# Performance work log

Hardware: AMD Instinct MI355X
Metric: run time of the kernel (lower is better)

The kernel has to match this reference:

```python
import jax, jax.numpy as jnp
import numpy as np
from jax import lax

IN_CH = 256
NUM_CLASSES = 21
ROI = 7
SCALE = 1.0 / 32
SR = 2  # sampling_ratio
B = 2
NPROP = 128
FH = FW = 32
IMG = 1024
SCORE_THRESH = 0.05
NMS_THRESH = 0.5
MAX_DET = 100


def setup_inputs() -> dict:
    key = jax.random.key(0)
    ks = jax.random.split(key, 10)
    features = jax.random.normal(ks[0], (B, IN_CH, FH, FW), jnp.float32)
    x1 = jax.random.uniform(ks[1], (B, NPROP), minval=0.0, maxval=IMG - 160.0)
    y1 = jax.random.uniform(ks[2], (B, NPROP), minval=0.0, maxval=IMG - 160.0)
    w = jax.random.uniform(ks[3], (B, NPROP), minval=32.0, maxval=160.0)
    h = jax.random.uniform(ks[4], (B, NPROP), minval=32.0, maxval=160.0)
    proposals = jnp.stack([x1, y1, x1 + w, y1 + h], axis=-1)  # [B, NPROP, 4]
    img_sizes = jnp.full((B, 2), IMG, dtype=jnp.int32)  # (h, w)
    feat_dim = IN_CH * ROI * ROI

    def kaiming(k, shape):
        return jax.random.normal(k, shape, jnp.float32) * np.float32(np.sqrt(2.0 / shape[1]))

    W1 = kaiming(ks[5], (1024, feat_dim)); b1 = jnp.zeros((1024,), jnp.float32)
    W2 = kaiming(ks[6], (1024, 1024)); b2 = jnp.zeros((1024,), jnp.float32)
    Wc = jax.random.normal(ks[7], (NUM_CLASSES, 1024), jnp.float32) * 0.01
    bc = jnp.zeros((NUM_CLASSES,), jnp.float32)
    Wb = jax.random.normal(ks[8], (NUM_CLASSES * 4, 1024), jnp.float32) * 0.001
    bb = jnp.zeros((NUM_CLASSES * 4,), jnp.float32)
    return dict(features=features, proposals=proposals, img_sizes=img_sizes,
                W1=W1, b1=b1, W2=W2, b2=b2, Wc=Wc, bc=bc, Wb=Wb, bb=bb)


def roi_align(features, bidx, rois):
    """torchvision-style RoIAlign (aligned=False), spatial_scale=SCALE, sampling_ratio=SR.
    features [B,C,H,W], bidx [N] int, rois [N,4] -> [N, C*ROI*ROI] (channel-major flatten)."""
    Bf, C, H, W = features.shape
    x1 = rois[:, 0] * SCALE; y1 = rois[:, 1] * SCALE
    x2 = rois[:, 2] * SCALE; y2 = rois[:, 3] * SCALE
    rw = jnp.maximum(x2 - x1, 1.0); rh = jnp.maximum(y2 - y1, 1.0)
    bw = rw / ROI; bh = rh / ROI
    # per-bin sample offsets: [ROI, SR]
    g = jnp.arange(ROI, dtype=jnp.float32)[:, None] + (jnp.arange(SR, dtype=jnp.float32)[None, :] + 0.5) / SR
    ys = y1[:, None, None] + g[None] * bh[:, None, None]  # [N, ROI, SR]
    xs = x1[:, None, None] + g[None] * bw[:, None, None]  # [N, ROI, SR]
    y = ys[:, :, :, None, None]  # [N,ph,sy,1,1]
    x = xs[:, None, None, :, :]  # [N,1,1,pw,sx]
    inb = (y >= -1.0) & (y <= H) & (x >= -1.0) & (x <= W)  # [N,ph,sy,pw,sx]
    yc = jnp.clip(y, 0.0, H - 1.0); xc = jnp.clip(x, 0.0, W - 1.0)
    y0f = jnp.floor(yc); x0f = jnp.floor(xc)
    y0 = y0f.astype(jnp.int32); x0 = x0f.astype(jnp.int32)
    y1i = jnp.minimum(y0 + 1, H - 1); x1i = jnp.minimum(x0 + 1, W - 1)
    ly = yc - y0f; lx = xc - x0f
    hy = 1.0 - ly; hx = 1.0 - lx
    b = bidx[:, None, None, None, None]
    # gather four corners: advanced indices broadcast -> [N,ph,sy,pw,sx,C]
    f00 = features[b, :, y0, x0]
    f01 = features[b, :, y0, x1i]
    f10 = features[b, :, y1i, x0]
    f11 = features[b, :, y1i, x1i]
    val = ((hy * hx)[..., None] * f00 + (hy * lx)[..., None] * f01
           + (ly * hx)[..., None] * f10 + (ly * lx)[..., None] * f11)
    val = val * inb[..., None]
    pooled = val.mean(axis=(2, 4))            # [N, ph, pw, C]
    pooled = jnp.transpose(pooled, (0, 3, 1, 2))  # [N, C, ph, pw] (torch layout)
    return pooled.reshape(pooled.shape[0], -1)


def decode_boxes(deltas, props):
    pw = props[..., 2] - props[..., 0]
    ph = props[..., 3] - props[..., 1]
    px = props[..., 0] + pw / 2
    py = props[..., 1] + ph / 2
    cx = px + deltas[..., 0] * pw
    cy = py + deltas[..., 1] * ph
    w = pw * jnp.exp(deltas[..., 2])
    h = ph * jnp.exp(deltas[..., 3])
    return jnp.stack([cx - w / 2, cy - h / 2, cx + w / 2, cy + h / 2], axis=-1)


def nms_fixed(boxes, scores, valid, iou_thresh, max_out):
    """Greedy NMS with fixed shapes. Returns (indices[max_out], ok_mask[max_out])."""
    M = scores.shape[0]
    s = jnp.where(valid, scores, -jnp.inf)
    order = jnp.argsort(-s)
    b = boxes[order]; v = valid[order]
    bx1, by1, bx2, by2 = b[:, 0], b[:, 1], b[:, 2], b[:, 3]
    area = (bx2 - bx1) * (by2 - by1)
    idxs = jnp.arange(M)

    def body(i, keep):
        xi1 = jnp.maximum(bx1[i], bx1); yi1 = jnp.maximum(by1[i], by1)
        xi2 = jnp.minimum(bx2[i], bx2); yi2 = jnp.minimum(by2[i], by2)
        inter = jnp.maximum(xi2 - xi1, 0.0) * jnp.maximum(yi2 - yi1, 0.0)
        iou = inter / (area[i] + area - inter + 1e-9)
        suppress = (iou > iou_thresh) & (idxs > i)
        return jnp.where(keep[i], keep & ~suppress, keep)

    keep = lax.fori_loop(0, M, body, v)
    pos = jnp.where(keep, idxs, M)
    take = jnp.sort(pos)[:max_out]
    ok = take < M
    take = jnp.where(ok, take, 0)
    return order[take], ok


def postprocess_image(probs, reg, props, img_hw):
    Ncls = probs.shape[1]
    scores = probs[:, 1:]                    # [N, C-1] (skip background)
    deltas = reg[:, 1:, :]                   # [N, C-1, 4]
    boxes = decode_boxes(deltas, props[:, None, :])  # [N, C-1, 4]
    h = img_hw[0].astype(boxes.dtype); w = img_hw[1].astype(boxes.dtype)
    boxes = jnp.stack([jnp.clip(boxes[..., 0], 0.0, w), jnp.clip(boxes[..., 1], 0.0, h),
                       jnp.clip(boxes[..., 2], 0.0, w), jnp.clip(boxes[..., 3], 0.0, h)], axis=-1)
    labels = jnp.broadcast_to(jnp.arange(1, Ncls, dtype=jnp.int32)[None, :], scores.shape)
    fb = boxes.reshape(-1, 4); fs = scores.reshape(-1); fl = labels.reshape(-1)
    valid = fs > SCORE_THRESH
    maxc = jnp.max(jnp.where(valid, jnp.max(fb, axis=1), 0.0))
    off = fl.astype(fb.dtype) * (maxc + 1.0)
    zero = jnp.zeros_like(off)
    fb_off = fb + jnp.stack([off, zero, off, zero], axis=-1)
    idx, ok = nms_fixed(fb_off, fs, valid, NMS_THRESH, MAX_DET)
    m = ok.astype(fb.dtype)
    return fb[idx] * m[:, None], fs[idx] * m, fl[idx] * ok.astype(jnp.int32)


def reference(features, proposals, img_sizes, W1, b1, W2, b2, Wc, bc, Wb, bb):
    Bn, NP = proposals.shape[0], proposals.shape[1]
    bidx = jnp.repeat(jnp.arange(Bn, dtype=jnp.int32), NP)
    props_flat = proposals.reshape(-1, 4)
    roi_feats = roi_align(features, bidx, props_flat)       # [N, C*49]
    x = jax.nn.relu(roi_feats @ W1.T + b1)
    x = jax.nn.relu(x @ W2.T + b2)
    cls_logits = x @ Wc.T + bc                              # [N, NUM_CLASSES]
    box_reg = (x @ Wb.T + bb).reshape(-1, NUM_CLASSES, 4)   # [N, NUM_CLASSES, 4]
    probs = jax.nn.softmax(cls_logits, axis=-1)
    out_b, out_s, out_l = [], [], []
    for i in range(Bn):
        p = probs[i * NP:(i + 1) * NP]
        r = box_reg[i * NP:(i + 1) * NP]
        bi, si, li = postprocess_image(p, r, proposals[i], img_sizes[i])
        out_b.append(bi); out_s.append(si); out_l.append(li)
    return jnp.stack(out_b), jnp.stack(out_s), jnp.stack(out_l)
```

## Files before the change

### kernel.cpp

```cpp
#include <hip/hip_runtime.h>
#include <math.h>

#define IN_CH   256
#define NCLS    21
#define ROIW    7
#define NPROP   128
#define BATCH   2
#define NROI    (BATCH*NPROP)
#define FEAT_DIM (IN_CH*ROIW*ROIW)
#define HID     1024
#define NCAND   (NPROP*(NCLS-1))
#define MAXDET  100
#define SCORE_T 0.05f
#define NMS_T   0.5f

__global__ __launch_bounds__(256) void transpose_feat(const float* __restrict__ feat,
                                                      float* __restrict__ ft) {
    int img = blockIdx.z;
    int cb = blockIdx.y;
    int pb = blockIdx.x;
    __shared__ float t[32][33];
    int tx = threadIdx.x & 31, ty = threadIdx.x >> 5;
#pragma unroll
    for (int i = 0; i < 4; ++i) {
        int c = ty + i * 8;
        t[c][tx] = feat[(size_t)img * 262144 + (size_t)(cb * 32 + c) * 1024 + pb * 32 + tx];
    }
    __syncthreads();
#pragma unroll
    for (int i = 0; i < 4; ++i) {
        int p = ty + i * 8;
        ft[(size_t)img * 262144 + (size_t)(pb * 32 + p) * 256 + cb * 32 + tx] = t[tx][p];
    }
}

__global__ __launch_bounds__(256) void roi_align_tr(const float* __restrict__ ft,
                                                    const float* __restrict__ props,
                                                    float* __restrict__ out) {
    int n = blockIdx.x >> 1;
    int half = blockIdx.x & 1;
    int img = n / NPROP;
    int q0 = half ? 25 : 0;
    int nq = half ? 24 : 25;
    const float* pr = props + n * 4;
    float x1 = pr[0] * 0.03125f, y1 = pr[1] * 0.03125f;
    float x2 = pr[2] * 0.03125f, y2 = pr[3] * 0.03125f;
    float rw = fmaxf(x2 - x1, 1.0f), rh = fmaxf(y2 - y1, 1.0f);
    float bw = rw / 7.0f, bh = rh / 7.0f;
    int cg = threadIdx.x & 63;
    int qg = threadIdx.x >> 6;
    __shared__ float tile[25][260];
    const float* base = ft + (size_t)img * 262144 + cg * 4;
    for (int j = qg; j < nq; j += 4) {
        int q = q0 + j;
        int iy = q / 7, ix = q % 7;
        float ax = 0.f, ay = 0.f, az = 0.f, aw = 0.f;
#pragma unroll
        for (int s = 0; s < 4; ++s) {
            int sy = s >> 1, sx = s & 1;
            float gy = (float)iy + ((float)sy + 0.5f) / 2.0f;
            float gx = (float)ix + ((float)sx + 0.5f) / 2.0f;
            float y = y1 + gy * bh;
            float x = x1 + gx * bw;
            bool inb = (y >= -1.0f) && (y <= 32.0f) && (x >= -1.0f) && (x <= 32.0f);
            float yc = fminf(fmaxf(y, 0.0f), 31.0f);
            float xc = fminf(fmaxf(x, 0.0f), 31.0f);
            float y0f = floorf(yc), x0f = floorf(xc);
            int y0 = (int)y0f, x0i = (int)x0f;
            int y1i = min(y0 + 1, 31), x1i = min(x0i + 1, 31);
            float ly = yc - y0f, lx = xc - x0f;
            float hy = 1.0f - ly, hx = 1.0f - lx;
            float wg = inb ? 1.0f : 0.0f;
            float w00 = hy * hx * wg, w01 = hy * lx * wg, w10 = ly * hx * wg, w11 = ly * lx * wg;
            float4 f00 = *(const float4*)(base + (size_t)(y0 * 32 + x0i) * 256);
            float4 f01 = *(const float4*)(base + (size_t)(y0 * 32 + x1i) * 256);
            float4 f10 = *(const float4*)(base + (size_t)(y1i * 32 + x0i) * 256);
            float4 f11 = *(const float4*)(base + (size_t)(y1i * 32 + x1i) * 256);
            ax += w00 * f00.x + w01 * f01.x + w10 * f10.x + w11 * f11.x;
            ay += w00 * f00.y + w01 * f01.y + w10 * f10.y + w11 * f11.y;
            az += w00 * f00.z + w01 * f01.z + w10 * f10.z + w11 * f11.z;
            aw += w00 * f00.w + w01 * f01.w + w10 * f10.w + w11 * f11.w;
        }
        *(float4*)&tile[j][cg * 4] = make_float4(ax * 0.25f, ay * 0.25f, az * 0.25f, aw * 0.25f);
    }
    __syncthreads();
    float* ob = out + (size_t)n * FEAT_DIM + q0;
    int tid = threadIdx.x;
    if (half == 0) {
        for (int i = tid; i < 256 * 25; i += 256) {
            int c = i / 25, ql = i % 25;
            ob[c * 49 + ql] = tile[ql][c];
        }
    } else {
        for (int i = tid; i < 256 * 24; i += 256) {
            int c = i / 24, ql = i % 24;
            ob[c * 49 + ql] = tile[ql][c];
        }
    }
}

#define GBM 128
#define GBN 128
#define GBK 16
__global__ __launch_bounds__(256) void gemm_tn_part(const float* __restrict__ A,
                                                    const float* __restrict__ Wt,
                                                    float* __restrict__ Cp,
                                                    int Nr, int Mo, int K) {
    const int S = gridDim.z;
    const int kchunk = K / S;
    const int k0 = blockIdx.z * kchunk;
    const int n0 = blockIdx.y * GBM;
    const int j0 = blockIdx.x * GBN;
    __shared__ float As[GBK][GBM + 4];
    __shared__ float Ws[GBK][GBN + 4];
    const int tid = threadIdx.x;
    const int tx = tid & 15;
    const int ty = tid >> 4;
    const int r0 = tx << 2;
    const int c0 = ty << 2;
    const int srow = tid >> 1;
    const int skk = (tid & 1) << 3;
    float acc[8][8];
#pragma unroll
    for (int r = 0; r < 8; ++r)
#pragma unroll
        for (int c = 0; c < 8; ++c) acc[r][c] = 0.0f;

    const int iters = kchunk / GBK;
    const float* Abase = A + (size_t)(n0 + srow) * K + skk;
    const float* Wbase = Wt + (size_t)(j0 + srow) * K + skk;
    float4 pa0 = *(const float4*)(Abase + k0);
    float4 pa1 = *(const float4*)(Abase + k0 + 4);
    float4 pw0 = *(const float4*)(Wbase + k0);
    float4 pw1 = *(const float4*)(Wbase + k0 + 4);

#pragma unroll 1
    for (int it = 0; it < iters; ++it) {
        __syncthreads();
        As[skk + 0][srow] = pa0.x; As[skk + 1][srow] = pa0.y; As[skk + 2][srow] = pa0.z; As[skk + 3][srow] = pa0.w;
        As[skk + 4][srow] = pa1.x; As[skk + 5][srow] = pa1.y; As[skk + 6][srow] = pa1.z; As[skk + 7][srow] = pa1.w;
        Ws[skk + 0][srow] = pw0.x; Ws[skk + 1][srow] = pw0.y; Ws[skk + 2][srow] = pw0.z; Ws[skk + 3][srow] = pw0.w;
        Ws[skk + 4][srow] = pw1.x; Ws[skk + 5][srow] = pw1.y; Ws[skk + 6][srow] = pw1.z; Ws[skk + 7][srow] = pw1.w;
        __syncthreads();
        if (it + 1 < iters) {
            int kc = k0 + (it + 1) * GBK;
            pa0 = *(const float4*)(Abase + kc);
            pa1 = *(const float4*)(Abase + kc + 4);
            pw0 = *(const float4*)(Wbase + kc);
            pw1 = *(const float4*)(Wbase + kc + 4);
        }
#pragma unroll
        for (int k = 0; k < GBK; ++k) {
            float4 t0 = *(const float4*)&As[k][r0];
            float4 t1 = *(const float4*)&As[k][r0 + 64];
            float4 u0 = *(const float4*)&Ws[k][c0];
            float4 u1 = *(const float4*)&Ws[k][c0 + 64];
            float a[8] = {t0.x, t0.y, t0.z, t0.w, t1.x, t1.y, t1.z, t1.w};
            float w[8] = {u0.x, u0.y, u0.z, u0.w, u1.x, u1.y, u1.z, u1.w};
#pragma unroll
            for (int r = 0; r < 8; ++r)
#pragma unroll
                for (int c = 0; c < 8; ++c)
                    acc[r][c] = fmaf(a[r], w[c], acc[r][c]);
        }
    }
#pragma unroll
    for (int r = 0; r < 8; ++r) {
        int gr = n0 + ((r < 4) ? (r0 + r) : (r0 + 64 + r - 4));
        float* o = Cp + ((size_t)blockIdx.z * Nr + gr) * Mo + j0;
        *(float4*)(o + c0)      = make_float4(acc[r][0], acc[r][1], acc[r][2], acc[r][3]);
        *(float4*)(o + c0 + 64) = make_float4(acc[r][4], acc[r][5], acc[r][6], acc[r][7]);
    }
}

__global__ __launch_bounds__(256) void reduce_bias_relu(const float* __restrict__ Cp,
                                                        const float* __restrict__ bias,
                                                        float* __restrict__ X,
                                                        int Nr, int Mo, int S) {
    int idx = blockIdx.x * 256 + threadIdx.x;
    int total = (Nr * Mo) >> 2;
    if (idx >= total) return;
    int e = idx << 2;
    int j = e % Mo;
    float4 s = make_float4(0.f, 0.f, 0.f, 0.f);
    for (int ss = 0; ss < S; ++ss) {
        float4 c = *(const float4*)(Cp + (size_t)ss * Nr * Mo + e);
        s.x += c.x; s.y += c.y; s.z += c.z; s.w += c.w;
    }
    float4 b = *(const float4*)(bias + j);
    s.x = fmaxf(s.x + b.x, 0.f); s.y = fmaxf(s.y + b.y, 0.f);
    s.z = fmaxf(s.z + b.z, 0.f); s.w = fmaxf(s.w + b.w, 0.f);
    *(float4*)(X + e) = s;
}

__global__ __launch_bounds__(256) void heads_k(const float* __restrict__ X2,
                                               const float* __restrict__ Wc, const float* __restrict__ bc,
                                               const float* __restrict__ Wb, const float* __restrict__ bb,
                                               float* __restrict__ probs, float* __restrict__ breg) {
    int n = blockIdx.x;
    int tid = threadIdx.x;
    __shared__ float xs[HID];
    __shared__ float lg[NCLS];
    __shared__ float ssum;
    *(float4*)&xs[tid * 4] = *(const float4*)(X2 + (size_t)n * HID + tid * 4);
    __syncthreads();
    int wave = tid >> 6, lane = tid & 63;
    for (int h = wave; h < 105; h += 4) {
        const float* w = (h < 21) ? (Wc + (size_t)h * HID) : (Wb + (size_t)(h - 21) * HID);
        float acc = 0.0f;
#pragma unroll
        for (int k0 = 0; k0 < HID; k0 += 256) {
            float4 wv = *(const float4*)(w + k0 + lane * 4);
            float4 xv = *(const float4*)&xs[k0 + lane * 4];
            acc = fmaf(wv.x, xv.x, acc);
            acc = fmaf(wv.y, xv.y, acc);
            acc = fmaf(wv.z, xv.z, acc);
            acc = fmaf(wv.w, xv.w, acc);
        }
#pragma unroll
        for (int m = 32; m; m >>= 1) acc += __shfl_xor(acc, m, 64);
        if (lane == 0) {
            if (h < 21) lg[h] = acc + bc[h];
            else breg[(size_t)n * 84 + (h - 21)] = acc + bb[h - 21];
        }
    }
    __syncthreads();
    if (tid == 0) {
        float m = lg[0];
        for (int c = 1; c < 21; ++c) m = fmaxf(m, lg[c]);
        float s = 0.0f;
        for (int c = 0; c < 21; ++c) { float e = expf(lg[c] - m); lg[c] = e; s += e; }
        ssum = s;
    }
    __syncthreads();
    if (tid < 21) probs[(size_t)n * 21 + tid] = lg[tid] / ssum;
}

__global__ __launch_bounds__(256) void cand_k(const float* __restrict__ props,
                                              const int* __restrict__ img_sizes,
                                              const float* __restrict__ probs,
                                              const float* __restrict__ breg,
                                              float* __restrict__ cbox,
                                              float* __restrict__ csc,
                                              unsigned long long* __restrict__ ckey,
                                              int* __restrict__ vcount) {
    int t = blockIdx.x * 256 + threadIdx.x;
    if (blockIdx.x == 0 && threadIdx.x < 2) vcount[threadIdx.x] = 0;
    if (t >= BATCH * NCAND) return;
    int img = t / NCAND, m = t % NCAND;
    int p = m / 20, c = m % 20 + 1;
    int row = img * NPROP + p;
    float s = probs[(size_t)row * 21 + c];
    const float* pr = props + row * 4;
    float pw = pr[2] - pr[0], ph = pr[3] - pr[1];
    float px = pr[0] + pw * 0.5f, py = pr[1] + ph * 0.5f;
    const float* d = breg + (size_t)row * 84 + c * 4;
    float cx = px + d[0] * pw;
    float cy = py + d[1] * ph;
    float w = pw * expf(d[2]);
    float h = ph * expf(d[3]);
    float bx1 = cx - w * 0.5f, by1 = cy - h * 0.5f, bx2 = cx + w * 0.5f, by2 = cy + h * 0.5f;
    float Wi = (float)img_sizes[img * 2 + 1], Hi = (float)img_sizes[img * 2 + 0];
    bx1 = fminf(fmaxf(bx1, 0.f), Wi); by1 = fminf(fmaxf(by1, 0.f), Hi);
    bx2 = fminf(fmaxf(bx2, 0.f), Wi); by2 = fminf(fmaxf(by2, 0.f), Hi);
    *(float4*)(cbox + (size_t)t * 4) = make_float4(bx1, by1, bx2, by2);
    csc[t] = s;
    bool valid = s > SCORE_T;
    unsigned int sb = __float_as_uint(s);
    ckey[t] = valid ? (((unsigned long long)sb << 32) | (unsigned int)(NCAND - 1 - m)) : 0ull;
}

__global__ __launch_bounds__(256) void rank_k(const float* __restrict__ cbox,
                                              const float* __restrict__ csc,
                                              const unsigned long long* __restrict__ ckey,
                                              float* __restrict__ sbox, float* __restrict__ ssc,
                                              int* __restrict__ sm, int* __restrict__ vcount) {
    int img = blockIdx.x / 40;
    int seg = blockIdx.x % 40;
    int base = img * NCAND;
    int lm = threadIdx.x & 63;
    int chunk = threadIdx.x >> 6;
    int m = seg * 64 + lm;
    __shared__ __align__(16) unsigned long long keys[NCAND];
    for (int j = threadIdx.x; j < NCAND; j += 256) keys[j] = ckey[base + j];
    unsigned long long mykey = ckey[base + m];
    float s = csc[base + m];
    bool valid = s > SCORE_T;
    __syncthreads();
    const ulonglong2* kp = (const ulonglong2*)&keys[chunk * 640];
    int r = 0;
#pragma unroll 4
    for (int j = 0; j < 320; ++j) {
        ulonglong2 kk = kp[j];
        r += (kk.x > mykey) ? 1 : 0;
        r += (kk.y > mykey) ? 1 : 0;
    }
    __shared__ int part[4][64];
    part[chunk][lm] = r;
    __syncthreads();
    if (chunk == 0) {
        int rank = part[0][lm] + part[1][lm] + part[2][lm] + part[3][lm];
        if (valid) {
            int o = base + rank;
            *(float4*)(sbox + (size_t)o * 4) = *(const float4*)(cbox + (size_t)(base + m) * 4);
            ssc[o] = s;
            sm[o] = m;
        }
    }
    int cnt = __syncthreads_count((chunk == 0) && valid);
    if (threadIdx.x == 0) atomicAdd(&vcount[img], cnt);
}

__global__ __launch_bounds__(64) void nms_k(const int* __restrict__ sm,
                                            const float* __restrict__ sbox,
                                            const int* __restrict__ vcount,
                                            int* __restrict__ skeep) {
    int bid = blockIdx.x;
    int img = bid / 20;
    int cls = bid % 20 + 1;
    int V = vcount[img];
    __shared__ float lx1[128], ly1[128], lx2[128], ly2[128];
    __shared__ int lpos[128];
    __shared__ int lcnt;
    __shared__ int keepL[128];
    int lane = threadIdx.x;
    if (lane == 0) lcnt = 0;
    __syncthreads();
    for (int p0 = 0; p0 < V; p0 += 64) {
        int p = p0 + lane;
        bool pred = false;
        if (p < V) {
            int m = sm[img * NCAND + p];
            pred = (m % 20 + 1) == cls;
        }
        unsigned long long mask = __ballot(pred);
        int base = lcnt;
        if (pred) {
            int idx = base + __popcll(mask & ((1ull << lane) - 1ull));
            const float* bx = sbox + (size_t)(img * NCAND + (p0 + lane)) * 4;
            lx1[idx] = bx[0]; ly1[idx] = bx[1]; lx2[idx] = bx[2]; ly2[idx] = bx[3];
            lpos[idx] = p0 + lane;
        }
        __syncthreads();
        if (lane == 0) lcnt += (int)__popcll(mask);
        __syncthreads();
    }
    int C = lcnt;
    for (int j = lane; j < 128; j += 64) keepL[j] = 1;
    __syncthreads();
    for (int i = 0; i < C; ++i) {
        __syncthreads();
        if (keepL[i] == 0) continue;
        float X1 = lx1[i], Y1 = ly1[i], X2 = lx2[i], Y2 = ly2[i];
        float ai = (X2 - X1) * (Y2 - Y1);
        for (int j = i + 1 + lane; j < C; j += 64) {
            if (keepL[j]) {
                float xi1 = fmaxf(X1, lx1[j]);
                float yi1 = fmaxf(Y1, ly1[j]);
                float xi2 = fminf(X2, lx2[j]);
                float yi2 = fminf(Y2, ly2[j]);
                float inter = fmaxf(xi2 - xi1, 0.f) * fmaxf(yi2 - yi1, 0.f);
                float aj = (lx2[j] - lx1[j]) * (ly2[j] - ly1[j]);
                float iou = inter / (ai + aj - inter + 1e-9f);
                if (iou > NMS_T) keepL[j] = 0;
            }
        }
    }
    __syncthreads();
    for (int j = lane; j < C; j += 64) skeep[img * NCAND + lpos[j]] = keepL[j];
}

__global__ __launch_bounds__(256) void write_k(const float* __restrict__ sbox,
                                               const float* __restrict__ ssc,
                                               const int* __restrict__ sm,
                                               const int* __restrict__ skeep,
                                               const int* __restrict__ vcount,
                                               float* __restrict__ out) {
    int img = blockIdx.x;
    int tid = threadIdx.x;
    float* ob = out + img * MAXDET * 4;
    float* os = out + BATCH * MAXDET * 4 + img * MAXDET;
    float* ol = out + BATCH * MAXDET * 5 + img * MAXDET;
    for (int i = tid; i < MAXDET * 4; i += 256) ob[i] = 0.0f;
    for (int i = tid; i < MAXDET; i += 256) { os[i] = 0.0f; ol[i] = 0.0f; }
    __syncthreads();
    int V = vcount[img];
    int chunk = (V + 255) / 256;
    int lo = tid * chunk, hi = min(lo + chunk, V);
    int cnt = 0;
    for (int p = lo; p < hi; ++p) cnt += skeep[img * NCAND + p];
    __shared__ int cs[256];
    __shared__ int pre[256];
    cs[tid] = cnt;
    __syncthreads();
    if (tid == 0) {
        int run = 0;
        for (int t = 0; t < 256; ++t) { pre[t] = run; run += cs[t]; }
    }
    __syncthreads();
    int r = pre[tid];
    for (int p = lo; p < hi; ++p) {
        if (skeep[img * NCAND + p]) {
            if (r < MAXDET) {
                const float* bx = sbox + (size_t)(img * NCAND + p) * 4;
                ob[r * 4 + 0] = bx[0]; ob[r * 4 + 1] = bx[1];
                ob[r * 4 + 2] = bx[2]; ob[r * 4 + 3] = bx[3];
                os[r] = ssc[img * NCAND + p];
                ol[r] = (float)(sm[img * NCAND + p] % 20 + 1);
            }
            ++r;
        }
    }
}

extern "C" void kernel_launch(void* const* d_in, const int* in_sizes, int n_in,
                              void* d_out, int out_size, void* d_ws, size_t ws_size,
                              hipStream_t stream) {
    const float* features  = (const float*)d_in[0];
    const float* proposals = (const float*)d_in[1];
    const int*   img_sizes = (const int*)d_in[2];
    const float* W1 = (const float*)d_in[3];
    const float* b1 = (const float*)d_in[4];
    const float* W2 = (const float*)d_in[5];
    const float* b2 = (const float*)d_in[6];
    const float* Wc = (const float*)d_in[7];
    const float* bc = (const float*)d_in[8];
    const float* Wb = (const float*)d_in[9];
    const float* bb = (const float*)d_in[10];
    float* out = (float*)d_out;

    float* ws = (float*)d_ws;
    float* roi   = ws;
    float* x1    = roi + 3211264;
    float* x2    = x1 + 262144;
    float* cpart = x2 + 262144;
    float* featT = cpart;
    float* probs = cpart + 4194304;
    float* breg  = probs + 5376;
    float* cbox  = breg + 21504;
    float* csc   = cbox + 20480;
    unsigned long long* ckey = (unsigned long long*)(csc + 5120);
    float* sbox  = csc + 5120 + 10240;
    float* ssc   = sbox + 20480;
    int*   sm    = (int*)(ssc + 5120);
    int*   skeep = sm + 5120;
    int*   vcnt  = skeep + 5120;

    hipLaunchKernelGGL(transpose_feat, dim3(32, 8, 2), dim3(256), 0, stream, features, featT);
    hipLaunchKernelGGL(roi_align_tr, dim3(NROI * 2), dim3(256), 0, stream, featT, proposals, roi);
    hipLaunchKernelGGL(gemm_tn_part, dim3(8, 2, 16), dim3(256), 0, stream, roi, W1, cpart, NROI, HID, FEAT_DIM);
    hipLaunchKernelGGL(reduce_bias_relu, dim3(256), dim3(256), 0, stream, cpart, b1, x1, NROI, HID, 16);
    hipLaunchKernelGGL(gemm_tn_part, dim3(8, 2, 16), dim3(256), 0, stream, x1, W2, cpart, NROI, HID, HID);
    hipLaunchKernelGGL(reduce_bias_relu, dim3(256), dim3(256), 0, stream, cpart, b2, x2, NROI, HID, 16);
    hipLaunchKernelGGL(heads_k, dim3(NROI), dim3(256), 0, stream, x2, Wc, bc, Wb, bb, probs, breg);
    hipLaunchKernelGGL(cand_k, dim3((BATCH * NCAND + 255) / 256), dim3(256), 0, stream,
                       proposals, img_sizes, probs, breg, cbox, csc, ckey, vcnt);
    hipLaunchKernelGGL(rank_k, dim3(80), dim3(256), 0, stream, cbox, csc, ckey, sbox, ssc, sm, vcnt);
    hipLaunchKernelGGL(nms_k, dim3(BATCH * 20), dim3(64), 0, stream, sm, sbox, vcnt, skeep);
    hipLaunchKernelGGL(write_k, dim3(BATCH), dim3(256), 0, stream, sbox, ssc, sm, skeep, vcnt, out);
}
```

Before: 323.5 us.

## Fuse second reduce, heads and candidate decode; double-buffer GEMM LDS fragments

Merges the second split-K reduction with bias+ReLU, the classification/box heads, softmax and candidate box decoding into one kernel. This removes two launches and the global round trips through x2, probs and breg. Separately, the GEMM inner loop now prefetches the next k-slice from shared memory into registers while computing the current one, to hide LDS latency. The prefetch adds register pressure to an already heavy 8x8 accumulator tile.

```diff
diff --git a/kernel.cpp b/kernel.cpp
--- a/kernel.cpp
+++ b/kernel.cpp
@@ -149,14 +149,24 @@
             pw0 = *(const float4*)(Wbase + kc);
             pw1 = *(const float4*)(Wbase + kc + 4);
         }
+        float4 fa0[2], fa1[2], fw0[2], fw1[2];
+        fa0[0] = *(const float4*)&As[0][r0];
+        fa1[0] = *(const float4*)&As[0][r0 + 64];
+        fw0[0] = *(const float4*)&Ws[0][c0];
+        fw1[0] = *(const float4*)&Ws[0][c0 + 64];
 #pragma unroll
         for (int k = 0; k < GBK; ++k) {
-            float4 t0 = *(const float4*)&As[k][r0];
-            float4 t1 = *(const float4*)&As[k][r0 + 64];
-            float4 u0 = *(const float4*)&Ws[k][c0];
-            float4 u1 = *(const float4*)&Ws[k][c0 + 64];
-            float a[8] = {t0.x, t0.y, t0.z, t0.w, t1.x, t1.y, t1.z, t1.w};
-            float w[8] = {u0.x, u0.y, u0.z, u0.w, u1.x, u1.y, u1.z, u1.w};
+            const int cur = k & 1, nxt = cur ^ 1;
+            if (k + 1 < GBK) {
+                fa0[nxt] = *(const float4*)&As[k + 1][r0];
+                fa1[nxt] = *(const float4*)&As[k + 1][r0 + 64];
+                fw0[nxt] = *(const float4*)&Ws[k + 1][c0];
+                fw1[nxt] = *(const float4*)&Ws[k + 1][c0 + 64];
+            }
+            float a[8] = {fa0[cur].x, fa0[cur].y, fa0[cur].z, fa0[cur].w,
+                          fa1[cur].x, fa1[cur].y, fa1[cur].z, fa1[cur].w};
+            float w[8] = {fw0[cur].x, fw0[cur].y, fw0[cur].z, fw0[cur].w,
+                          fw1[cur].x, fw1[cur].y, fw1[cur].z, fw1[cur].w};
 #pragma unroll
             for (int r = 0; r < 8; ++r)
 #pragma unroll
@@ -193,16 +203,36 @@
     *(float4*)(X + e) = s;
 }
 
-__global__ __launch_bounds__(256) void heads_k(const float* __restrict__ X2,
-                                               const float* __restrict__ Wc, const float* __restrict__ bc,
-                                               const float* __restrict__ Wb, const float* __restrict__ bb,
-                                               float* __restrict__ probs, float* __restrict__ breg) {
+__global__ __launch_bounds__(256) void heads_cand_k(const float* __restrict__ Cp2,
+                                                    const float* __restrict__ b2,
+                                                    const float* __restrict__ Wc, const float* __restrict__ bc,
+                                                    const float* __restrict__ Wb, const float* __restrict__ bb,
+                                                    const float* __restrict__ props,
+                                                    const int* __restrict__ img_sizes,
+                                                    float* __restrict__ cbox,
+                                                    float* __restrict__ csc,
+                                                    unsigned long long* __restrict__ ckey,
+                                                    int* __restrict__ vcount) {
     int n = blockIdx.x;
     int tid = threadIdx.x;
+    if (n == 0 && tid < 2) vcount[tid] = 0;
     __shared__ float xs[HID];
     __shared__ float lg[NCLS];
+    __shared__ float bs[84];
     __shared__ float ssum;
-    *(float4*)&xs[tid * 4] = *(const float4*)(X2 + (size_t)n * HID + tid * 4);
+    {
+        int e = n * HID + tid * 4;
+        float4 s = make_float4(0.f, 0.f, 0.f, 0.f);
+#pragma unroll
+        for (int ss = 0; ss < 16; ++ss) {
+            float4 c = *(const float4*)(Cp2 + (size_t)ss * (NROI * HID) + e);
+            s.x += c.x; s.y += c.y; s.z += c.z; s.w += c.w;
+        }
+        float4 b = *(const float4*)(b2 + tid * 4);
+        s.x = fmaxf(s.x + b.x, 0.f); s.y = fmaxf(s.y + b.y, 0.f);
+        s.z = fmaxf(s.z + b.z, 0.f); s.w = fmaxf(s.w + b.w, 0.f);
+        *(float4*)&xs[tid * 4] = s;
+    }
     __syncthreads();
     int wave = tid >> 6, lane = tid & 63;
     for (int h = wave; h < 105; h += 4) {
@@ -221,7 +251,7 @@
         for (int m = 32; m; m >>= 1) acc += __shfl_xor(acc, m, 64);
         if (lane == 0) {
             if (h < 21) lg[h] = acc + bc[h];
-            else breg[(size_t)n * 84 + (h - 21)] = acc + bb[h - 21];
+            else bs[h - 21] = acc + bb[h - 21];
         }
     }
     __syncthreads();
@@ -233,41 +263,30 @@
         ssum = s;
     }
     __syncthreads();
-    if (tid < 21) probs[(size_t)n * 21 + tid] = lg[tid] / ssum;
-}
-
-__global__ __launch_bounds__(256) void cand_k(const float* __restrict__ props,
-                                              const int* __restrict__ img_sizes,
-                                              const float* __restrict__ probs,
-                                              const float* __restrict__ breg,
-                                              float* __restrict__ cbox,
-                                              float* __restrict__ csc,
-                                              unsigned long long* __restrict__ ckey,
-                                              int* __restrict__ vcount) {
-    int t = blockIdx.x * 256 + threadIdx.x;
-    if (blockIdx.x == 0 && threadIdx.x < 2) vcount[threadIdx.x] = 0;
-    if (t >= BATCH * NCAND) return;
-    int img = t / NCAND, m = t % NCAND;
-    int p = m / 20, c = m % 20 + 1;
-    int row = img * NPROP + p;
-    float s = probs[(size_t)row * 21 + c];
-    const float* pr = props + row * 4;
-    float pw = pr[2] - pr[0], ph = pr[3] - pr[1];
-    float px = pr[0] + pw * 0.5f, py = pr[1] + ph * 0.5f;
-    const float* d = breg + (size_t)row * 84 + c * 4;
-    float cx = px + d[0] * pw;
-    float cy = py + d[1] * ph;
-    float w = pw * expf(d[2]);
-    float h = ph * expf(d[3]);
-    float bx1 = cx - w * 0.5f, by1 = cy - h * 0.5f, bx2 = cx + w * 0.5f, by2 = cy + h * 0.5f;
-    float Wi = (float)img_sizes[img * 2 + 1], Hi = (float)img_sizes[img * 2 + 0];
-    bx1 = fminf(fmaxf(bx1, 0.f), Wi); by1 = fminf(fmaxf(by1, 0.f), Hi);
-    bx2 = fminf(fmaxf(bx2, 0.f), Wi); by2 = fminf(fmaxf(by2, 0.f), Hi);
-    *(float4*)(cbox + (size_t)t * 4) = make_float4(bx1, by1, bx2, by2);
-    csc[t] = s;
-    bool valid = s > SCORE_T;
-    unsigned int sb = __float_as_uint(s);
-    ckey[t] = valid ? (((unsigned long long)sb << 32) | (unsigned int)(NCAND - 1 - m)) : 0ull;
+    if (tid < 20) {
+        int c = tid + 1;
+        int img = n / NPROP;
+        float s = lg[c] / ssum;
+        const float* pr = props + n * 4;
+        float pw = pr[2] - pr[0], ph = pr[3] - pr[1];
+        float px = pr[0] + pw * 0.5f, py = pr[1] + ph * 0.5f;
+        const float* d = &bs[c * 4];
+        float cx = px + d[0] * pw;
+        float cy = py + d[1] * ph;
+        float w = pw * expf(d[2]);
+        float h = ph * expf(d[3]);
+        float bx1 = cx - w * 0.5f, by1 = cy - h * 0.5f, bx2 = cx + w * 0.5f, by2 = cy + h * 0.5f;
+        float Wi = (float)img_sizes[img * 2 + 1], Hi = (float)img_sizes[img * 2 + 0];
+        bx1 = fminf(fmaxf(bx1, 0.f), Wi); by1 = fminf(fmaxf(by1, 0.f), Hi);
+        bx2 = fminf(fmaxf(bx2, 0.f), Wi); by2 = fminf(fmaxf(by2, 0.f), Hi);
+        int t = n * 20 + tid;
+        *(float4*)(cbox + (size_t)t * 4) = make_float4(bx1, by1, bx2, by2);
+        csc[t] = s;
+        bool valid = s > SCORE_T;
+        unsigned int sb = __float_as_uint(s);
+        int m = t - img * NCAND;
+        ckey[t] = valid ? (((unsigned long long)sb << 32) | (unsigned int)(NCAND - 1 - m)) : 0ull;
+    }
 }
 
 __global__ __launch_bounds__(256) void rank_k(const float* __restrict__ cbox,
@@ -432,12 +451,9 @@
     float* ws = (float*)d_ws;
     float* roi   = ws;
     float* x1    = roi + 3211264;
-    float* x2    = x1 + 262144;
-    float* cpart = x2 + 262144;
+    float* cpart = x1 + 262144;
     float* featT = cpart;
-    float* probs = cpart + 4194304;
-    float* breg  = probs + 5376;
-    float* cbox  = breg + 21504;
+    float* cbox  = cpart + 16 * 262144;
     float* csc   = cbox + 20480;
     unsigned long long* ckey = (unsigned long long*)(csc + 5120);
     float* sbox  = csc + 5120 + 10240;
@@ -451,10 +467,8 @@
     hipLaunchKernelGGL(gemm_tn_part, dim3(8, 2, 16), dim3(256), 0, stream, roi, W1, cpart, NROI, HID, FEAT_DIM);
     hipLaunchKernelGGL(reduce_bias_relu, dim3(256), dim3(256), 0, stream, cpart, b1, x1, NROI, HID, 16);
     hipLaunchKernelGGL(gemm_tn_part, dim3(8, 2, 16), dim3(256), 0, stream, x1, W2, cpart, NROI, HID, HID);
-    hipLaunchKernelGGL(reduce_bias_relu, dim3(256), dim3(256), 0, stream, cpart, b2, x2, NROI, HID, 16);
-    hipLaunchKernelGGL(heads_k, dim3(NROI), dim3(256), 0, stream, x2, Wc, bc, Wb, bb, probs, breg);
-    hipLaunchKernelGGL(cand_k, dim3((BATCH * NCAND + 255) / 256), dim3(256), 0, stream,
-                       proposals, img_sizes, probs, breg, cbox, csc, ckey, vcnt);
+    hipLaunchKernelGGL(heads_cand_k, dim3(NROI), dim3(256), 0, stream, cpart, b2, Wc, bc, Wb, bb,
+                       proposals, img_sizes, cbox, csc, ckey, vcnt);
     hipLaunchKernelGGL(rank_k, dim3(80), dim3(256), 0, stream, cbox, csc, ckey, sbox, ssc, sm, vcnt);
     hipLaunchKernelGGL(nms_k, dim3(BATCH * 20), dim3(64), 0, stream, sm, sbox, vcnt, skeep);
     hipLaunchKernelGGL(write_k, dim3(BATCH), dim3(256), 0, stream, sbox, ssc, sm, skeep, vcnt, out);
```

Measured after the change: 319.9 us. About the same (-1.1%).
